# Kernel optimization log

Measured on AMD Instinct MI355X. Metric: run time of the kernel, lower is better.

Reference implementation:

```python
import jax, jax.numpy as jnp
import numpy as np

IN_FEATURES = 1024
OUT_FEATURES = 1024
N = 8192

def setup_inputs() -> dict:
    key = jax.random.key(0)
    kx, kw, kb = jax.random.split(key, 3)
    x = jax.random.normal(kx, (N, IN_FEATURES), dtype=jnp.float32)
    # nn.Linear default init: U(-1/sqrt(in), 1/sqrt(in))
    bound = 1.0 / np.sqrt(IN_FEATURES)
    W = jax.random.uniform(kw, (OUT_FEATURES, IN_FEATURES), minval=-bound, maxval=bound, dtype=jnp.float32)
    b = jax.random.uniform(kb, (OUT_FEATURES,), minval=-bound, maxval=bound, dtype=jnp.float32)
    return {"x": x, "W": W, "b": b}

def reference(x, W, b):
    # h: [N, D]
    h = x @ W.T + b
    # scores: [N, N]; tanh applied to raw scores, softmax over dim=1 (rows)
    scores = jnp.tanh(h @ h.T)
    attn = jax.nn.softmax(scores, axis=1)
    out = jnp.tanh(attn @ h)
    return out
```

## Files before the change

kernel.cpp:

```cpp
#include <hip/hip_runtime.h>
#include <hip/hip_bf16.h>
#include <cstdint>
#include <cstddef>

typedef __bf16 bf16_t;
typedef __bf16 bf16x4 __attribute__((ext_vector_type(4)));
typedef __bf16 bf16x8 __attribute__((ext_vector_type(8)));
typedef float f32x4 __attribute__((ext_vector_type(4)));
typedef float f32x16 __attribute__((ext_vector_type(16)));
typedef float f32x2 __attribute__((ext_vector_type(2)));
typedef int i32x4 __attribute__((ext_vector_type(4)));
typedef int i32x8 __attribute__((ext_vector_type(8)));

#define NROWS 8192
#define DFEAT 1024
#define BK 32
#define NBLK 64
#define TILE_B (128 * BK)
#define F8TILE 8192
#define NTRI (NBLK * (NBLK + 1) / 2)

typedef __attribute__((address_space(3))) unsigned int lds_uint;
typedef __attribute__((address_space(1))) const unsigned int glb_uint;

__device__ __forceinline__ float fast_tanh(float x) {
  float e = __expf(2.0f * x);
  return 1.0f - 2.0f * __builtin_amdgcn_rcpf(e + 1.0f);
}

__device__ __forceinline__ unsigned pack_fp8x4(float a, float b, float c, float d) {
  unsigned v = 0;
  v = __builtin_amdgcn_cvt_pk_fp8_f32(a, b, v, false);
  v = __builtin_amdgcn_cvt_pk_fp8_f32(c, d, v, true);
  return v;
}

__global__ __launch_bounds__(256) void cast_kernel(const float* __restrict__ in,
                                                   bf16_t* __restrict__ out, int n4) {
  int i = blockIdx.x * 256 + threadIdx.x;
  if (i < n4) {
    float4 v = *(const float4*)(in + i * 4);
    bf16x4 o = {(bf16_t)v.x, (bf16_t)v.y, (bf16_t)v.z, (bf16_t)v.w};
    *(bf16x4*)(out + i * 4) = o;
  }
}

__device__ __forceinline__ void stage_async(const bf16_t* __restrict__ g, int ld,
                                            int row0, int k0, bf16_t* lds,
                                            int wave, int lane) {
#pragma unroll
  for (int t = 0; t < 2; ++t) {
    const int rb = (t * 4 + wave) * 16;
    const bf16_t* gp = g + (size_t)(row0 + rb + (lane >> 2)) * ld + (k0 + (lane & 3) * 8);
    __builtin_amdgcn_global_load_lds((glb_uint*)gp, (lds_uint*)(lds + rb * BK), 16, 0, 0);
  }
}

__device__ __forceinline__ void stage_f8(const uint8_t* __restrict__ g, int ld,
                                         int row0, int k0, uint8_t* lds,
                                         int wave, int lane) {
#pragma unroll
  for (int t = 0; t < 2; ++t) {
    const int rb = (t * 4 + wave) * 16;
    const uint8_t* gp = g + (size_t)(row0 + rb + (lane >> 2)) * ld + (k0 + (lane & 3) * 16);
    __builtin_amdgcn_global_load_lds((glb_uint*)gp, (lds_uint*)(lds + rb * 64), 16, 0, 0);
  }
}

__global__ __launch_bounds__(256) void gemm1_kernel(const bf16_t* __restrict__ xb,
                                                    const bf16_t* __restrict__ Wb,
                                                    const float* __restrict__ bias,
                                                    bf16_t* __restrict__ hout,
                                                    uint8_t* __restrict__ hT8) {
  __shared__ __align__(16) bf16_t smem[4 * TILE_B];
  const int tid = threadIdx.x;
  const int wave = tid >> 6, lane = tid & 63;
  const int wm = wave >> 1, wn = wave & 1;
  const int l15 = lane & 15, quad = lane >> 4;
  const int m0 = blockIdx.x * 128, n0 = blockIdx.y * 128;
  f32x4 acc[4][4] = {};
  const int NIT = DFEAT / BK;
  stage_async(xb, DFEAT, m0, 0, smem, wave, lane);
  stage_async(Wb, DFEAT, n0, 0, smem + TILE_B, wave, lane);
  __syncthreads();
  for (int it = 0; it < NIT; ++it) {
    bf16_t* lA = smem + (it & 1) * 2 * TILE_B;
    bf16_t* lB = lA + TILE_B;
    if (it + 1 < NIT) {
      bf16_t* nA = smem + ((it + 1) & 1) * 2 * TILE_B;
      stage_async(xb, DFEAT, m0, (it + 1) * BK, nA, wave, lane);
      stage_async(Wb, DFEAT, n0, (it + 1) * BK, nA + TILE_B, wave, lane);
    }
    bf16x8 a[4], b[4];
#pragma unroll
    for (int f = 0; f < 4; ++f) {
      a[f] = *(const bf16x8*)(lA + (wm * 64 + f * 16 + l15) * BK + quad * 8);
      b[f] = *(const bf16x8*)(lB + (wn * 64 + f * 16 + l15) * BK + quad * 8);
    }
#pragma unroll
    for (int i = 0; i < 4; ++i)
#pragma unroll
      for (int j = 0; j < 4; ++j)
        acc[i][j] = __builtin_amdgcn_mfma_f32_16x16x32_bf16(a[i], b[j], acc[i][j], 0, 0, 0);
    __syncthreads();
  }
#pragma unroll
  for (int i = 0; i < 4; ++i) {
    int rbase = m0 + wm * 64 + i * 16 + quad * 4;
#pragma unroll
    for (int j = 0; j < 4; ++j) {
      int col = n0 + wn * 64 + j * 16 + l15;
      float bv = bias[col];
      float hv[4];
#pragma unroll
      for (int r = 0; r < 4; ++r) hv[r] = acc[i][j][r] + bv;
#pragma unroll
      for (int r = 0; r < 4; ++r)
        hout[(size_t)(rbase + r) * DFEAT + col] = (bf16_t)hv[r];
      *(unsigned*)(hT8 + (size_t)col * NROWS + rbase) =
          pack_fp8x4(hv[0], hv[1], hv[2], hv[3]);
    }
  }
}

__global__ __launch_bounds__(256) void scores_sym_kernel(const bf16_t* __restrict__ h,
                                                         uint8_t* __restrict__ P,
                                                         float* __restrict__ lsum) {
  __shared__ __align__(16) char smem[4 * TILE_B * 2];
  uint8_t (*mir)[144] = (uint8_t(*)[144])smem;

  const int k = (int)blockIdx.x & 7;
  const int s = (int)blockIdx.x >> 3;
  int I, J, r, c;
  if (s < 36) {
    I = J = k;
    int tt = s; r = 0;
    while (tt >= 8 - r) { tt -= 8 - r; ++r; }
    c = r + tt;
  } else {
    int e, t;
    if (s < 228) { e = 3 * k + (s - 36) / 64; t = (s - 36) & 63; }
    else { e = 24 + (k >> 1); t = ((k & 1) << 5) + (s - 228); }
    int ee = e; I = 0;
    while (ee >= 7 - I) { ee -= 7 - I; ++I; }
    J = I + 1 + ee;
    r = t >> 3; c = t & 7;
  }
  const int bm = I * 8 + r, bn = J * 8 + c;
  const bool offdiag = (bm != bn);
  const int m0 = bm * 128, n0 = bn * 128;

  const int tid = threadIdx.x;
  const int wave = tid >> 6, lane = tid & 63;
  const int wm = wave >> 1, wn = wave & 1;
  const int l15 = lane & 15, quad = lane >> 4;

  f32x4 acc[4][4] = {};
  const int NIT = DFEAT / BK;
  stage_async(h, DFEAT, m0, 0, (bf16_t*)smem, wave, lane);
  stage_async(h, DFEAT, n0, 0, (bf16_t*)smem + TILE_B, wave, lane);
  __syncthreads();
  for (int it = 0; it < NIT; ++it) {
    bf16_t* lA = (bf16_t*)smem + (it & 1) * 2 * TILE_B;
    bf16_t* lB = lA + TILE_B;
    if (it + 1 < NIT) {
      bf16_t* nA = (bf16_t*)smem + ((it + 1) & 1) * 2 * TILE_B;
      stage_async(h, DFEAT, m0, (it + 1) * BK, nA, wave, lane);
      stage_async(h, DFEAT, n0, (it + 1) * BK, nA + TILE_B, wave, lane);
    }
    bf16x8 a[4], b[4];
#pragma unroll
    for (int f = 0; f < 4; ++f) {
      a[f] = *(const bf16x8*)(lA + (wm * 64 + f * 16 + l15) * BK + quad * 8);
      b[f] = *(const bf16x8*)(lB + (wn * 64 + f * 16 + l15) * BK + quad * 8);
    }
#pragma unroll
    for (int i = 0; i < 4; ++i)
#pragma unroll
      for (int j = 0; j < 4; ++j)
        acc[i][j] = __builtin_amdgcn_mfma_f32_16x16x32_bf16(a[i], b[j], acc[i][j], 0, 0, 0);
    __syncthreads();
  }

  float rs[4][4];
  float cs[4];
#pragma unroll
  for (int i = 0; i < 4; ++i)
#pragma unroll
    for (int r2 = 0; r2 < 4; ++r2) rs[i][r2] = 0.f;
#pragma unroll
  for (int j = 0; j < 4; ++j) cs[j] = 0.f;

#pragma unroll
  for (int i = 0; i < 4; ++i) {
    const int rl_loc = wm * 64 + i * 16 + quad * 4;
    const int rbase = m0 + rl_loc;
#pragma unroll
    for (int j = 0; j < 4; ++j) {
      const int cl_loc = wn * 64 + j * 16 + l15;
      const int col = n0 + cl_loc;
      float p[4];
#pragma unroll
      for (int r2 = 0; r2 < 4; ++r2) p[r2] = __expf(fast_tanh(acc[i][j][r2]));
      unsigned packed = pack_fp8x4(p[0], p[1], p[2], p[3]);
      f32x2 d0 = __builtin_amdgcn_cvt_pk_f32_fp8(packed, false);
      f32x2 d1 = __builtin_amdgcn_cvt_pk_f32_fp8(packed, true);
      float q[4] = {d0.x, d0.y, d1.x, d1.y};
#pragma unroll
      for (int r2 = 0; r2 < 4; ++r2) {
        rs[i][r2] += q[r2];
        cs[j] += q[r2];
        P[(size_t)(rbase + r2) * NROWS + col] = (uint8_t)(packed >> (8 * r2));
      }
      if (offdiag) *(unsigned*)&mir[cl_loc][rl_loc] = packed;
    }
  }

#pragma unroll
  for (int off = 1; off < 16; off <<= 1)
#pragma unroll
    for (int i = 0; i < 4; ++i)
#pragma unroll
      for (int r2 = 0; r2 < 4; ++r2) rs[i][r2] += __shfl_xor(rs[i][r2], off, 64);
  if (l15 == 0) {
#pragma unroll
    for (int i = 0; i < 4; ++i) {
      int rbase = m0 + wm * 64 + i * 16 + quad * 4;
#pragma unroll
      for (int r2 = 0; r2 < 4; ++r2) atomicAdd(&lsum[rbase + r2], rs[i][r2]);
    }
  }

  if (offdiag) {
#pragma unroll
    for (int off = 16; off < 64; off <<= 1)
#pragma unroll
      for (int j = 0; j < 4; ++j) cs[j] += __shfl_xor(cs[j], off, 64);
    if (quad == 0) {
#pragma unroll
      for (int j = 0; j < 4; ++j)
        atomicAdd(&lsum[n0 + wn * 64 + j * 16 + l15], cs[j]);
    }
    __syncthreads();
#pragma unroll
    for (int it = 0; it < 4; ++it) {
      int q2 = tid + it * 256;
      int c2 = q2 >> 3, r0 = (q2 & 7) * 16;
      uint4 v = *(const uint4*)(&mir[c2][r0]);
      *(uint4*)(P + (size_t)(n0 + c2) * NROWS + m0 + r0) = v;
    }
  }
}

__global__ __launch_bounds__(256) void pv_kernel(const uint8_t* __restrict__ P,
                                                 const uint8_t* __restrict__ hT8,
                                                 const float* __restrict__ lsum,
                                                 float* __restrict__ out) {
  __shared__ __align__(16) uint8_t smem[4 * F8TILE];
  const int tid = threadIdx.x;
  const int wave = tid >> 6, lane = tid & 63;
  const int wm = wave >> 1, wn = wave & 1;
  const int l31 = lane & 31, khalf = lane >> 5;
  const int m0 = blockIdx.x * 128, n0 = blockIdx.y * 128;
  f32x16 acc[2][2] = {};
  const int NIT = NROWS / 64;
  stage_f8(P, NROWS, m0, 0, smem, wave, lane);
  stage_f8(hT8, NROWS, n0, 0, smem + F8TILE, wave, lane);
  __syncthreads();
  for (int it = 0; it < NIT; ++it) {
    uint8_t* lA = smem + (it & 1) * 2 * F8TILE;
    uint8_t* lB = lA + F8TILE;
    if (it + 1 < NIT) {
      uint8_t* nA = smem + ((it + 1) & 1) * 2 * F8TILE;
      stage_f8(P, NROWS, m0, (it + 1) * 64, nA, wave, lane);
      stage_f8(hT8, NROWS, n0, (it + 1) * 64, nA + F8TILE, wave, lane);
    }
    i32x8 a[2], b[2];
#pragma unroll
    for (int f = 0; f < 2; ++f) {
      {
        int off = (wm * 64 + f * 32 + l31) * 64 + khalf * 32;
        i32x4 lo = *(const i32x4*)(lA + off);
        i32x4 hi = *(const i32x4*)(lA + off + 16);
        a[f] = i32x8{lo[0], lo[1], lo[2], lo[3], hi[0], hi[1], hi[2], hi[3]};
      }
      {
        int off = (wn * 64 + f * 32 + l31) * 64 + khalf * 32;
        i32x4 lo = *(const i32x4*)(lB + off);
        i32x4 hi = *(const i32x4*)(lB + off + 16);
        b[f] = i32x8{lo[0], lo[1], lo[2], lo[3], hi[0], hi[1], hi[2], hi[3]};
      }
    }
#pragma unroll
    for (int bi = 0; bi < 2; ++bi)
#pragma unroll
      for (int bj = 0; bj < 2; ++bj)
        acc[bi][bj] = __builtin_amdgcn_mfma_scale_f32_32x32x64_f8f6f4(
            a[bi], b[bj], acc[bi][bj], 0, 0, 0, 0x7F7F7F7F, 0, 0x7F7F7F7F);
    __syncthreads();
  }
#pragma unroll
  for (int bi = 0; bi < 2; ++bi)
#pragma unroll
    for (int bj = 0; bj < 2; ++bj) {
      int cbase = n0 + wn * 64 + bj * 32 + l31;
#pragma unroll
      for (int reg = 0; reg < 16; ++reg) {
        int row = m0 + wm * 64 + bi * 32 + (reg & 3) + 8 * (reg >> 2) + 4 * khalf;
        float rl = __builtin_amdgcn_rcpf(lsum[row]);
        out[(size_t)row * DFEAT + cbase] = fast_tanh(acc[bi][bj][reg] * rl);
      }
    }
}

extern "C" void kernel_launch(void* const* d_in, const int* in_sizes, int n_in,
                              void* d_out, int out_size, void* d_ws, size_t ws_size,
                              hipStream_t stream) {
  const float* x = (const float*)d_in[0];
  const float* W = (const float*)d_in[1];
  const float* bias = (const float*)d_in[2];
  float* out = (float*)d_out;

  bf16_t* xb = (bf16_t*)d_ws;
  bf16_t* Wb = xb + (size_t)NROWS * DFEAT;
  bf16_t* h  = Wb + (size_t)DFEAT * DFEAT;
  uint8_t* hT8 = (uint8_t*)(h + (size_t)NROWS * DFEAT);
  float* lsum = (float*)(hT8 + (size_t)DFEAT * NROWS);
  uint8_t* P = (uint8_t*)(lsum + NROWS);

  cast_kernel<<<(NROWS * DFEAT / 4) / 256, 256, 0, stream>>>(x, xb, NROWS * DFEAT / 4);
  cast_kernel<<<(DFEAT * DFEAT / 4) / 256, 256, 0, stream>>>(W, Wb, DFEAT * DFEAT / 4);
  gemm1_kernel<<<dim3(NROWS / 128, DFEAT / 128), 256, 0, stream>>>(xb, Wb, bias, h, hT8);
  hipMemsetAsync(lsum, 0, NROWS * sizeof(float), stream);
  scores_sym_kernel<<<NTRI, 256, 0, stream>>>(h, P, lsum);
  pv_kernel<<<dim3(NROWS / 128, DFEAT / 128), 256, 0, stream>>>(P, hT8, lsum, out);
}
```

Before: 325.9 us.

## Load scores GEMM operands directly from global into registers, dropping LDS staging

The symmetric scores kernel no longer stages h tiles into double-buffered LDS. Each wave now loads its MFMA fragments straight from global memory into registers, with a one-step register prefetch and no per-iteration barrier. Shared memory shrinks to just the mirror buffer, which can allow higher occupancy. In exchange, global loads are redundant across waves (each row fragment is fetched by two waves) and are 16-byte strided per lane, so the kernel leans more on L1/L2 bandwidth and latency hiding.

```diff
diff --git a/kernel.cpp b/kernel.cpp
--- a/kernel.cpp
+++ b/kernel.cpp
@@ -126,8 +126,7 @@
 __global__ __launch_bounds__(256) void scores_sym_kernel(const bf16_t* __restrict__ h,
                                                          uint8_t* __restrict__ P,
                                                          float* __restrict__ lsum) {
-  __shared__ __align__(16) char smem[4 * TILE_B * 2];
-  uint8_t (*mir)[144] = (uint8_t(*)[144])smem;
+  __shared__ __align__(16) uint8_t mir[128][144];
 
   const int k = (int)blockIdx.x & 7;
   const int s = (int)blockIdx.x >> 3;
@@ -155,31 +154,37 @@
   const int wm = wave >> 1, wn = wave & 1;
   const int l15 = lane & 15, quad = lane >> 4;
 
+  const bf16_t* ga = h + (size_t)(m0 + wm * 64 + l15) * DFEAT + quad * 8;
+  const bf16_t* gb = h + (size_t)(n0 + wn * 64 + l15) * DFEAT + quad * 8;
+
   f32x4 acc[4][4] = {};
   const int NIT = DFEAT / BK;
-  stage_async(h, DFEAT, m0, 0, (bf16_t*)smem, wave, lane);
-  stage_async(h, DFEAT, n0, 0, (bf16_t*)smem + TILE_B, wave, lane);
-  __syncthreads();
+  bf16x8 a[4], b[4];
+#pragma unroll
+  for (int f = 0; f < 4; ++f) {
+    a[f] = *(const bf16x8*)(ga + f * 16 * DFEAT);
+    b[f] = *(const bf16x8*)(gb + f * 16 * DFEAT);
+  }
+#pragma unroll 2
   for (int it = 0; it < NIT; ++it) {
-    bf16_t* lA = (bf16_t*)smem + (it & 1) * 2 * TILE_B;
-    bf16_t* lB = lA + TILE_B;
+    bf16x8 an[4], bn[4];
     if (it + 1 < NIT) {
-      bf16_t* nA = (bf16_t*)smem + ((it + 1) & 1) * 2 * TILE_B;
-      stage_async(h, DFEAT, m0, (it + 1) * BK, nA, wave, lane);
-      stage_async(h, DFEAT, n0, (it + 1) * BK, nA + TILE_B, wave, lane);
-    }
-    bf16x8 a[4], b[4];
-#pragma unroll
-    for (int f = 0; f < 4; ++f) {
-      a[f] = *(const bf16x8*)(lA + (wm * 64 + f * 16 + l15) * BK + quad * 8);
-      b[f] = *(const bf16x8*)(lB + (wn * 64 + f * 16 + l15) * BK + quad * 8);
+      const int k1 = (it + 1) * BK;
+#pragma unroll
+      for (int f = 0; f < 4; ++f) {
+        an[f] = *(const bf16x8*)(ga + f * 16 * DFEAT + k1);
+        bn[f] = *(const bf16x8*)(gb + f * 16 * DFEAT + k1);
+      }
     }
 #pragma unroll
     for (int i = 0; i < 4; ++i)
 #pragma unroll
       for (int j = 0; j < 4; ++j)
         acc[i][j] = __builtin_amdgcn_mfma_f32_16x16x32_bf16(a[i], b[j], acc[i][j], 0, 0, 0);
-    __syncthreads();
+    if (it + 1 < NIT) {
+#pragma unroll
+      for (int f = 0; f < 4; ++f) { a[f] = an[f]; b[f] = bn[f]; }
+    }
   }
 
   float rs[4][4];
```

New measurement: 455.4 us. 1.4x slower.
